# Kernel tuning notes

Hardware: AMD Instinct MI355X
Metric: run time of the kernel (lower is better)

## Reference

```python
import math
import jax, jax.numpy as jnp
import numpy as np

BLOCK = 32          # MRA block size (fixed to 32 by the CUDA kernels)
NUM_HEADS = 12
HEAD_DIM = 64
NUM_BLOCKS = 512    # top-k blocks kept per (batch*head) row
FIRST_N = 0         # initial_prior_first_n_blocks
DIAG_N = 3          # initial_prior_diagonal_n_blocks


def _low_res_logit(q, k, v, mask):
    # q,k,v: (B, S, D); mask: (B, S)
    B, S, D = q.shape
    nb = S // BLOCK
    tc = mask.reshape(B, nb, BLOCK).sum(-1)            # token count per block
    denom = tc[:, :, None] + 1e-6
    q_hat = q.reshape(B, nb, BLOCK, D).sum(2) / denom
    k_hat = k.reshape(B, nb, BLOCK, D).sum(2) / denom
    v_hat = v.reshape(B, nb, BLOCK, D).sum(2) / denom
    logit = jnp.einsum('bnd,bmd->bnm', q_hat, k_hat) / math.sqrt(D)
    row_max = logit.max(-1, keepdims=True)             # before mask penalty, as in torch
    logit = logit - 1e4 * ((tc[:, None, :] * tc[:, :, None]) < 0.5).astype(logit.dtype)
    return logit, tc, row_max, v_hat


def _block_idxes(lrl):
    # lrl: (B, nb, nb) normalized low-res logits (stop-gradient'ed by caller)
    B, nb, _ = lrl.shape
    if DIAG_N > 0:
        off = DIAG_N // 2
        r = jnp.arange(nb)
        diag = (jnp.abs(r[:, None] - r[None, :]) <= off).astype(lrl.dtype)
        lrl = lrl + diag[None] * 5000.0
    if FIRST_N > 0:
        lrl = lrl.at[:, :FIRST_N, :].add(5000.0)
        lrl = lrl.at[:, :, :FIRST_N].add(5000.0)
    vals, idx = jax.lax.top_k(lrl.reshape(B, -1), NUM_BLOCKS)
    thresh = vals.min(-1)
    hi_mask = (lrl >= thresh[:, None, None]).astype(lrl.dtype)
    return idx, hi_mask


def mra2_attention(q, k, v, mask):
    # q,k,v: (meta_batch, S, D); mask: (meta_batch, S). approx_mode == 'full'.
    B, S, D = q.shape
    nb = S // BLOCK
    q = q * mask[:, :, None]
    k = k * mask[:, :, None]
    v = v * mask[:, :, None]
    lrl, tc, row_max, v_hat = _low_res_logit(q, k, v, mask)
    idx, hi_mask = _block_idxes(jax.lax.stop_gradient(lrl - row_max))
    qi = idx // nb                                     # (B, NUM_BLOCKS) query block id
    ki = idx % nb                                      # (B, NUM_BLOCKS) key block id
    b_ix = jnp.arange(B)[:, None]
    # mm_to_sparse: gather blocks, block layout is (key_pos, query_pos) as in the CUDA kernel
    qb = q.reshape(B, nb, BLOCK, D)[b_ix, qi]          # (B, NB, 32, D)
    kb = k.reshape(B, nb, BLOCK, D)[b_ix, ki]
    hr_logit = jnp.einsum('bnkd,bnqd->bnkq', kb, qb) / math.sqrt(D)
    # sparse_max: per-query-row max over all selected blocks in that row
    idx_vals = hr_logit.max(-2)                        # (B, NB, 32q)
    max_vals = jnp.full((B, nb, BLOCK), -1e9, hr_logit.dtype).at[b_ix, qi].max(idx_vals)
    hr_logit = hr_logit - max_vals[b_ix, qi][:, :, None, :]
    # sparse_mask over key positions of each selected block
    mk = mask.reshape(B, nb, BLOCK)[b_ix, ki]          # (B, NB, 32k)
    hr_logit = hr_logit - 1e4 * (1.0 - mk)[:, :, :, None]
    hr_attn = jnp.exp(hr_logit)
    # sparse_dense_mm: scatter-add block contributions back to query rows
    vb = v.reshape(B, nb, BLOCK, D)[b_ix, ki]
    out_blk = jnp.einsum('bnkq,bnkd->bnqd', hr_attn, vb)
    hr_out = jnp.zeros((B, nb, BLOCK, D), q.dtype).at[b_ix, qi].add(out_blk).reshape(B, S, D)
    hr_norm = jnp.zeros((B, nb, BLOCK), q.dtype).at[b_ix, qi].add(hr_attn.sum(-2)).reshape(B, S)
    max_vals_flat = max_vals.reshape(B, S)
    # low-resolution branch (approx_mode == 'full')
    lr_attn = jnp.exp(lrl - row_max - 1e4 * hi_mask) * tc[:, None, :]
    lr_out = jnp.broadcast_to(
        jnp.einsum('bnm,bmd->bnd', lr_attn, v_hat)[:, :, None, :], (B, nb, BLOCK, D)
    ).reshape(B, S, D)
    lr_norm = jnp.broadcast_to(lr_attn.sum(-1)[:, :, None], (B, nb, BLOCK)).reshape(B, S)
    log_corr = (jnp.broadcast_to(row_max, (B, nb, BLOCK)).reshape(B, S) - max_vals_flat) * mask
    lr_corr = jnp.exp(log_corr * (log_corr <= 0).astype(log_corr.dtype))
    hr_corr = jnp.exp(-log_corr * (log_corr > 0).astype(log_corr.dtype))
    num = hr_out * hr_corr[:, :, None] + lr_out * lr_corr[:, :, None]
    den = hr_norm * hr_corr + lr_norm * lr_corr + 1e-6
    ctx = num / den[:, :, None]
    return ctx * mask[:, :, None]


def setup_inputs() -> dict:
    key = jax.random.key(0)
    ks = jax.random.split(key, 4)
    B, S, H = 4, 4096, 768
    return {
        'hidden_states': jax.random.normal(ks[0], (B, S, H), jnp.float32),
        'attention_mask': jnp.zeros((B, S), jnp.float32),  # extended mask form (0 == keep)
        'Wq': jax.random.normal(ks[1], (H, H), jnp.float32) * 0.02,
        'bq': jnp.zeros((H,), jnp.float32),
        'Wk': jax.random.normal(ks[2], (H, H), jnp.float32) * 0.02,
        'bk': jnp.zeros((H,), jnp.float32),
        'Wv': jax.random.normal(ks[3], (H, H), jnp.float32) * 0.02,
        'bv': jnp.zeros((H,), jnp.float32),
    }


def reference(hidden_states, attention_mask, Wq, bq, Wk, bk, Wv, bv):
    B, S, H = hidden_states.shape

    def heads(x):  # (B,S,H) -> (B*nh, S, hd)
        return x.reshape(B, S, NUM_HEADS, HEAD_DIM).transpose(0, 2, 1, 3).reshape(B * NUM_HEADS, S, HEAD_DIM)

    q = heads(hidden_states @ Wq.T + bq)
    k = heads(hidden_states @ Wk.T + bk)
    v = heads(hidden_states @ Wv.T + bv)
    # revert get_extended_attention_mask: (1 - m) * -10000 -> m
    mask = 1.0 + attention_mask / 10000.0
    mask = jnp.broadcast_to(mask[:, None, :], (B, NUM_HEADS, S)).reshape(B * NUM_HEADS, S)
    ctx = mra2_attention(q, k, v, mask)
    return ctx.reshape(B, NUM_HEADS, S, HEAD_DIM).transpose(0, 2, 1, 3).reshape(B, S, H)
```

## Files before the change

kernel.cpp:

```cpp
#include <hip/hip_runtime.h>
#include <math.h>


#define S_LEN 4096
#define NBLK  128
#define BHT   48
#define HD    64

typedef __attribute__((ext_vector_type(8))) short bf16x8;
typedef __attribute__((ext_vector_type(4))) float f32x4;
typedef unsigned short u16;
typedef unsigned int   u32;
typedef unsigned long long u64;

__device__ __forceinline__ u16 bf16rne(float x) {
    u32 u = __float_as_uint(x);
    u32 r = u + 0x7FFFu + ((u >> 16) & 1u);
    return (u16)(r >> 16);
}
__device__ __forceinline__ float b2f(u16 h) {
    return __uint_as_float((u32)h << 16);
}

__device__ __forceinline__ void gload_lds16(const void* g, void* l) {
    __builtin_amdgcn_global_load_lds((const __attribute__((address_space(1))) void*)g,
                                     (__attribute__((address_space(3))) void*)l, 16, 0, 0);
}

#define NX8 (16384 * 768 / 8)
#define NW8 (768 * 768 / 8)

__global__ __launch_bounds__(256) void split_all(
    const float* __restrict__ X,
    const float* __restrict__ Wq, const float* __restrict__ Wk, const float* __restrict__ Wv,
    u16* __restrict__ Xh, u16* __restrict__ Xl,
    u16* __restrict__ Wh, u16* __restrict__ Wl)
{
    int i = blockIdx.x * 256 + threadIdx.x;
    if (i >= NX8 + 3 * NW8) return;
    const float* src; u16* dh; u16* dl; size_t off8;
    if (i < NX8) { src = X; dh = Xh; dl = Xl; off8 = i; }
    else {
        int j = i - NX8;
        int w = j / NW8, r = j - w * NW8;
        src = (w == 0) ? Wq : (w == 1) ? Wk : Wv;
        dh = Wh + (size_t)w * 768 * 768;
        dl = Wl + (size_t)w * 768 * 768;
        off8 = r;
    }
    const float4* xp = (const float4*)src + off8 * 2;
    float4 a = xp[0], b = xp[1];
    float xs[8] = {a.x, a.y, a.z, a.w, b.x, b.y, b.z, b.w};
    bf16x8 vh, vl;
    #pragma unroll
    for (int j = 0; j < 8; ++j) {
        u16 hh = bf16rne(xs[j]);
        float hf = b2f(hh);
        vh[j] = (short)hh;
        vl[j] = (short)bf16rne(xs[j] - hf);
    }
    *(bf16x8*)&dh[off8 * 8] = vh;
    *(bf16x8*)&dl[off8 * 8] = vl;
}

__global__ __launch_bounds__(256, 3) void qkv_mfma(
    const u16* __restrict__ Xh, const u16* __restrict__ Xl,
    const u16* __restrict__ Wh, const u16* __restrict__ Wl,
    const float* __restrict__ bq, const float* __restrict__ bk, const float* __restrict__ bv,
    const float* __restrict__ am,
    u16* __restrict__ Qh, u16* __restrict__ Ql,
    u16* __restrict__ Kh, u16* __restrict__ Kl,
    u16* __restrict__ Vth, u16* __restrict__ Vtl)
{
    const int wg = blockIdx.x;
    const int logical = (wg & 7) * 288 + (wg >> 3);
    const int mt = logical / 18;
    const int rr = logical - mt * 18;
    const int nt = rr % 6;
    const int z  = rr / 6;

    const float* bias = (z == 0) ? bq : (z == 1) ? bk : bv;
    const u16* Wzh = Wh + (size_t)z * 768 * 768;
    const u16* Wzl = Wl + (size_t)z * 768 * 768;
    const int m0 = mt * 128, n0 = nt * 128;

    __shared__ char smem[32768];
    const int tid  = threadIdx.x;
    const int lane = tid & 63;
    const int w    = tid >> 6;
    const int wm   = (w >> 1) * 64, wn = (w & 1) * 64;

    const int rbase = (w < 2) ? m0 : n0;
    const int sub0  = (w & 1) * 4;
    char* ldsdst    = (w < 2) ? smem : (smem + 16384);
    const int srow = lane >> 2;
    const int scg  = (lane & 3) ^ ((lane >> 3) & 3);
    const int tslot = (lane & 15) * 4 + ((lane >> 4) ^ ((lane >> 1) & 3));

    f32x4 acc[4][4];
    #pragma unroll
    for (int i = 0; i < 4; ++i)
        #pragma unroll
        for (int j = 0; j < 4; ++j) acc[i][j] = (f32x4){0.f, 0.f, 0.f, 0.f};

    for (int k0 = 0; k0 < 2304; k0 += 64) {
        const u16* srcA = (k0 < 1536) ? Xh : Xl;
        const u16* srcB = (k0 < 768) ? Wzh : ((k0 < 1536) ? Wzl : Wzh);
        const int  kk   = (k0 < 768) ? k0 : ((k0 < 1536) ? (k0 - 768) : (k0 - 1536));
        const u16* src  = (w < 2) ? srcA : srcB;
        __syncthreads();
        #pragma unroll
        for (int h = 0; h < 2; ++h)
            #pragma unroll
            for (int i = 0; i < 4; ++i) {
                int sub = sub0 + i;
                const u16* g = src + (size_t)(rbase + sub * 16 + srow) * 768
                                   + (kk + h * 32 + scg * 8);
                gload_lds16(g, ldsdst + (h * 8 + sub) * 1024);
            }
        __syncthreads();

        #pragma unroll
        for (int h = 0; h < 2; ++h) {
            bf16x8 af[4], bf[4];
            #pragma unroll
            for (int f = 0; f < 4; ++f) {
                af[f] = *(const bf16x8*)&smem[(h * 8 + (w >> 1) * 4 + f) * 1024 + tslot * 16];
                bf[f] = *(const bf16x8*)&smem[16384 + (h * 8 + (w & 1) * 4 + f) * 1024 + tslot * 16];
            }
            #pragma unroll
            for (int i = 0; i < 4; ++i)
                #pragma unroll
                for (int j = 0; j < 4; ++j)
                    acc[i][j] = __builtin_amdgcn_mfma_f32_16x16x32_bf16(af[i], bf[j], acc[i][j], 0, 0, 0);
        }
    }

    if (z < 2) {
        u16* Ph = (z == 0) ? Qh : Kh;
        u16* Pl = (z == 0) ? Ql : Kl;
        const float qscale = (z == 0) ? 0.125f : 1.0f;
        #pragma unroll
        for (int i = 0; i < 4; ++i) {
            #pragma unroll
            for (int j = 0; j < 4; ++j) {
                int col = n0 + wn + j * 16 + (lane & 15);
                int h = col >> 6, d = col & 63;
                float bsv = bias[col];
                #pragma unroll
                for (int r = 0; r < 4; ++r) {
                    int row = m0 + wm + i * 16 + (lane >> 4) * 4 + r;
                    int b = row >> 12, s = row & 4095;
                    float mv = 1.0f + am[row] * 1e-4f;
                    float e = (acc[i][j][r] + bsv) * mv * qscale;
                    u16 hh = bf16rne(e);
                    u16 ll = bf16rne(e - b2f(hh));
                    size_t a = (((size_t)(b * 12 + h)) * S_LEN + s) * HD + d;
                    Ph[a] = hh; Pl[a] = ll;
                }
            }
        }
    } else {
        u32* buf = (u32*)smem;
        const int bb = m0 >> 12;
        #pragma unroll
        for (int p = 0; p < 4; ++p) {
            const int hh_ = p & 1;
            const int rh  = p >> 1;
            __syncthreads();
            if (((w & 1) == hh_) && ((w >> 1) == rh)) {
                #pragma unroll
                for (int i = 0; i < 4; ++i) {
                    #pragma unroll
                    for (int j = 0; j < 4; ++j) {
                        int d_local = j * 16 + (lane & 15);
                        int col = n0 + hh_ * 64 + d_local;
                        float bsv = bias[col];
                        #pragma unroll
                        for (int r = 0; r < 4; ++r) {
                            int s_local = i * 16 + (lane >> 4) * 4 + r;
                            float mv = 1.0f + am[m0 + rh * 64 + s_local] * 1e-4f;
                            float e = (acc[i][j][r] + bsv) * mv;
                            u16 h16 = bf16rne(e);
                            u16 l16 = bf16rne(e - b2f(h16));
                            buf[d_local * 66 + s_local] = ((u32)h16 << 16) | (u32)l16;
                        }
                    }
                }
            }
            __syncthreads();
            int d_local = tid >> 2;
            int s_chunk = (tid & 3) * 16;
            int head = (n0 >> 6) + hh_;
            size_t ob = (((size_t)(bb * 12 + head)) * HD + d_local) * S_LEN
                        + (m0 & 4095) + rh * 64 + s_chunk;
            #pragma unroll
            for (int gq = 0; gq < 2; ++gq) {
                bf16x8 vh8, vl8;
                #pragma unroll
                for (int t = 0; t < 8; ++t) {
                    u32 pk = buf[d_local * 66 + s_chunk + gq * 8 + t];
                    vh8[t] = (short)(pk >> 16);
                    vl8[t] = (short)(pk & 0xFFFF);
                }
                *(bf16x8*)&Vth[ob + gq * 8] = vh8;
                *(bf16x8*)&Vtl[ob + gq * 8] = vl8;
            }
        }
    }
}

__global__ __launch_bounds__(256) void hsum_kernel(
    const float* __restrict__ X, const float* __restrict__ am,
    double* __restrict__ hsum, double* __restrict__ tcd)
{
    int blk = blockIdx.x & 127, b = blockIdx.x >> 7;
    int tid = threadIdx.x;
    const float* xb  = X  + ((size_t)(b * S_LEN + blk * 32)) * 768;
    const float* amb = am + b * S_LEN + blk * 32;
    for (int d = tid; d < 768; d += 256) {
        double s = 0.0;
        for (int t = 0; t < 32; ++t)
            s += (double)xb[(size_t)t * 768 + d] * (1.0 + (double)amb[t] * 1e-4);
        hsum[(size_t)blockIdx.x * 768 + d] = s;
    }
    if (tid == 0) {
        double t = 0.0;
        for (int i = 0; i < 32; ++i) t += 1.0 + (double)amb[i] * 1e-4;
        tcd[blockIdx.x] = t;
    }
}

__global__ __launch_bounds__(256) void ghat_kernel(
    const double* __restrict__ hsum,
    const float* __restrict__ Wq, const float* __restrict__ Wk,
    const float* __restrict__ bq, const float* __restrict__ bk,
    const double* __restrict__ tcd,
    double* __restrict__ qhat, double* __restrict__ khat)
{
    const float* W; const float* bias; double* outp;
    if (blockIdx.z == 0) { W = Wq; bias = bq; outp = qhat; }
    else                 { W = Wk; bias = bk; outp = khat; }
    const int n0 = blockIdx.x * 64, m0 = blockIdx.y * 64;
    __shared__ double As[16][72];
    __shared__ float  Bs[16][72];
    const int tid = threadIdx.x;
    const int tx = tid & 15, ty = tid >> 4;
    double acc[4][4] = {};
    const int lr = tid >> 2, lc = (tid & 3) * 4;
    for (int k0 = 0; k0 < 768; k0 += 16) {
        double a0 = hsum[(size_t)(m0 + lr) * 768 + k0 + lc + 0];
        double a1 = hsum[(size_t)(m0 + lr) * 768 + k0 + lc + 1];
        double a2 = hsum[(size_t)(m0 + lr) * 768 + k0 + lc + 2];
        double a3 = hsum[(size_t)(m0 + lr) * 768 + k0 + lc + 3];
        float4 bv = *(const float4*)&W[(size_t)(n0 + lr) * 768 + k0 + lc];
        __syncthreads();
        As[lc+0][lr] = a0; As[lc+1][lr] = a1; As[lc+2][lr] = a2; As[lc+3][lr] = a3;
        Bs[lc+0][lr] = bv.x; Bs[lc+1][lr] = bv.y; Bs[lc+2][lr] = bv.z; Bs[lc+3][lr] = bv.w;
        __syncthreads();
        #pragma unroll
        for (int kk = 0; kk < 16; ++kk) {
            double af[4]; float bf[4];
            #pragma unroll
            for (int i = 0; i < 4; ++i) af[i] = As[kk][ty*4+i];
            #pragma unroll
            for (int j = 0; j < 4; ++j) bf[j] = Bs[kk][tx*4+j];
            #pragma unroll
            for (int i = 0; i < 4; ++i)
                #pragma unroll
                for (int j = 0; j < 4; ++j)
                    acc[i][j] += af[i] * (double)bf[j];
        }
    }
    #pragma unroll
    for (int i = 0; i < 4; ++i) {
        int m = m0 + ty*4 + i;
        int b = m >> 7, blk = m & 127;
        double t = tcd[m];
        #pragma unroll
        for (int j = 0; j < 4; ++j) {
            int o = n0 + tx*4 + j;
            int h = o >> 6, d = o & 63;
            outp[(((size_t)(b*12 + h)) * NBLK + blk) * HD + d] = (acc[i][j] + t * (double)bias[o]) / (t + 1e-6);
        }
    }
}

__global__ __launch_bounds__(128) void lrl_kernel(
    const double* __restrict__ qhat, const double* __restrict__ khat,
    const double* __restrict__ tcd,
    double* __restrict__ lrl, double* __restrict__ rmax,
    u64* __restrict__ keys)
{
    const int qi = blockIdx.x, bh = blockIdx.y;
    const int b = bh / 12;
    __shared__ double qr[64];
    __shared__ double red[128];
    const int tid = threadIdx.x;
    if (tid < 64) qr[tid] = qhat[(((size_t)bh) * NBLK + qi) * HD + tid];
    __syncthreads();
    const double* kr = &khat[(((size_t)bh) * NBLK + tid) * HD];
    double s = 0.0;
    #pragma unroll
    for (int d = 0; d < 64; d += 2) {
        double2 kv2 = *(const double2*)&kr[d];
        s += qr[d] * kv2.x + qr[d + 1] * kv2.y;
    }
    s *= 0.125;
    red[tid] = s;
    __syncthreads();
    for (int off = 64; off > 0; off >>= 1) {
        if (tid < off) red[tid] = fmax(red[tid], red[tid + off]);
        __syncthreads();
    }
    const double rmaxv = red[0];
    double pen = (tcd[b * NBLK + qi] * tcd[b * NBLK + tid] < 0.5) ? 1e4 : 0.0;
    const double lv = s - pen;
    lrl[(size_t)bh * (NBLK*NBLK) + (size_t)qi * NBLK + tid] = lv;
    if (tid == 0) rmax[bh * NBLK + qi] = rmaxv;
    int dd = qi - tid; if (dd < 0) dd = -dd;
    double ks_ = lv - rmaxv + ((dd <= 1) ? 5000.0 : 0.0);
    u64 u = (u64)__double_as_longlong(ks_);
    u = (u >> 63) ? ~u : (u | 0x8000000000000000ULL);
    keys[(size_t)bh * (NBLK*NBLK) + (size_t)qi * NBLK + tid] = u;
}

__global__ __launch_bounds__(64) void vhat_kernel(
    const u16* __restrict__ Vth, const u16* __restrict__ Vtl,
    const double* __restrict__ tcd,
    float* __restrict__ vhat, float* __restrict__ tcf)
{
    const int d = blockIdx.x, bh = blockIdx.y;
    const int b = bh / 12;
    const int l = threadIdx.x;
    const u16* ph = Vth + ((size_t)bh * HD + d) * S_LEN + l * 64;
    const u16* pl = Vtl + ((size_t)bh * HD + d) * S_LEN + l * 64;
    float s[2] = {0.f, 0.f};
    #pragma unroll
    for (int g = 0; g < 2; ++g) {
        #pragma unroll
        for (int v = 0; v < 4; ++v) {
            bf16x8 vh = *(const bf16x8*)&ph[g * 32 + v * 8];
            bf16x8 vl = *(const bf16x8*)&pl[g * 32 + v * 8];
            #pragma unroll
            for (int j = 0; j < 8; ++j)
                s[g] += b2f((u16)vh[j]) + b2f((u16)vl[j]);
        }
    }
    #pragma unroll
    for (int g = 0; g < 2; ++g) {
        int blk = l * 2 + g;
        float tc = (float)tcd[b * NBLK + blk];
        vhat[(((size_t)bh) * NBLK + blk) * HD + d] = s[g] / (tc + 1e-6f);
        if (d == 0) tcf[bh * NBLK + blk] = tc;
    }
}

__global__ __launch_bounds__(256) void topk_kernel(
    const u64* __restrict__ keys,
    double* __restrict__ th64, int* __restrict__ cnt, unsigned char* __restrict__ lists,
    int* __restrict__ eqbuf, int* __restrict__ eqcnt)
{
    const int bh = blockIdx.x, tid = threadIdx.x;
    const int wid = tid >> 6;
    __shared__ int hist[4][256];
    __shared__ u64 s_pref;
    __shared__ int s_K;
    const u64* kp = keys + (size_t)bh * (NBLK*NBLK);
    if (tid < 128) cnt[bh * NBLK + tid] = 0;
    if (tid == 0) eqcnt[bh] = 0;

    u64 pref = 0, pmask = 0;
    int K = 512;
    for (int by = 7; by >= 0; --by) {
        #pragma unroll
        for (int w = 0; w < 4; ++w) hist[w][tid] = 0;
        __syncthreads();
        for (int i = tid; i < NBLK*NBLK; i += 256) {
            u64 u = kp[i];
            if ((u & pmask) == pref)
                atomicAdd(&hist[wid][(int)((u >> (by*8)) & 255)], 1);
        }
        __syncthreads();
        int tot = hist[0][tid] + hist[1][tid] + hist[2][tid] + hist[3][tid];
        hist[0][tid] = tot;
        __syncthreads();
        if (tid == 0) {
            int c = 0, bsel = 0;
            for (int x = 255; x >= 0; --x) {
                if (c + hist[0][x] >= K) { bsel = x; break; }
                c += hist[0][x];
            }
            s_pref = pref | ((u64)bsel << (by*8));
            s_K = K - c;
        }
        __syncthreads();
        pref = s_pref; K = s_K;
        pmask |= 0xFFULL << (by*8);
        __syncthreads();
    }
    const u64 tkey = pref;
    int n_take = K;
    if (tid == 0) {
        u64 u = (tkey & 0x8000000000000000ULL) ? (tkey ^ 0x8000000000000000ULL) : ~tkey;
        th64[bh] = __longlong_as_double((long long)u);
    }
    for (int i = tid; i < NBLK*NBLK; i += 256) {
        u64 u = kp[i];
        if (u > tkey) {
            int qi = i >> 7, ki = i & 127;
            int pos = atomicAdd(&cnt[bh * NBLK + qi], 1);
            lists[(((size_t)bh) * NBLK + qi) * NBLK + pos] = (unsigned char)ki;
        } else if (u == tkey) {
            int e = atomicAdd(&eqcnt[bh], 1);
            if (e < 512) eqbuf[bh * 512 + e] = i;
        }
    }
    __syncthreads();
    if (tid == 0) {
        int ne = eqcnt[bh]; if (ne > 512) ne = 512;
        int* eb = &eqbuf[bh * 512];
        for (int a = 1; a < ne; ++a) {
            int v = eb[a]; int x = a - 1;
            while (x >= 0 && eb[x] > v) { eb[x+1] = eb[x]; --x; }
            eb[x+1] = v;
        }
        if (n_take > ne) n_take = ne;
        for (int j = 0; j < n_take; ++j) {
            int i = eb[j]; int qi = i >> 7, ki = i & 127;
            int pos = cnt[bh * NBLK + qi]++;
            lists[(((size_t)bh) * NBLK + qi) * NBLK + pos] = (unsigned char)ki;
        }
    }
    __syncthreads();
    if (tid < 128) {
        int n = cnt[bh * NBLK + tid];
        unsigned char* l = &lists[(((size_t)bh) * NBLK + tid) * NBLK];
        for (int a = 1; a < n; ++a) {
            unsigned char v = l[a]; int x = a - 1;
            while (x >= 0 && l[x] > v) { l[x+1] = l[x]; --x; }
            l[x+1] = v;
        }
    }
}

__global__ __launch_bounds__(64) void hr_mfma(
    const u16* __restrict__ Qh, const u16* __restrict__ Ql,
    const u16* __restrict__ Kh, const u16* __restrict__ Kl,
    const u16* __restrict__ Vth, const u16* __restrict__ Vtl,
    const double* __restrict__ lrl64, const double* __restrict__ rmax64, const double* __restrict__ th64,
    const int* __restrict__ cnt, const unsigned char* __restrict__ lists,
    const float* __restrict__ vhat, const float* __restrict__ tcf,
    const float* __restrict__ am, float* __restrict__ out)
{
    const int qi = blockIdx.x, bh = blockIdx.y;
    const int l  = threadIdx.x;
    const int lr_ = l & 15, lg = l >> 4;
    __shared__ u16 PhL[32][40];
    __shared__ u16 PlL[32][40];
    __shared__ float wlr[128];
    __shared__ float lrvec[64];

    bf16x8 qfh[2][2], qfl[2][2];
    #pragma unroll
    for (int qs = 0; qs < 2; ++qs)
        #pragma unroll
        for (int ds = 0; ds < 2; ++ds) {
            size_t a = (((size_t)bh) * S_LEN + qi * 32 + qs * 16 + lr_) * HD + ds * 32 + lg * 8;
            qfh[qs][ds] = *(const bf16x8*)&Qh[a];
            qfl[qs][ds] = *(const bf16x8*)&Ql[a];
        }

    float m_run[2][4], l_run[2][4];
    f32x4 oacc[2][4];
    #pragma unroll
    for (int qs = 0; qs < 2; ++qs) {
        #pragma unroll
        for (int r = 0; r < 4; ++r) { m_run[qs][r] = -1e30f; l_run[qs][r] = 0.f; }
        #pragma unroll
        for (int dv = 0; dv < 4; ++dv) oacc[qs][dv] = (f32x4){0.f, 0.f, 0.f, 0.f};
    }

    const int c = cnt[bh * NBLK + qi];
    const unsigned char* ml = &lists[(((size_t)bh) * NBLK + qi) * NBLK];

    for (int bi = 0; bi < c; ++bi) {
        const int ki = ml[bi];
        f32x4 S[2][2];
        #pragma unroll
        for (int qs = 0; qs < 2; ++qs)
            #pragma unroll
            for (int ks = 0; ks < 2; ++ks) S[qs][ks] = (f32x4){0.f, 0.f, 0.f, 0.f};
        #pragma unroll
        for (int ds = 0; ds < 2; ++ds)
            #pragma unroll
            for (int ks = 0; ks < 2; ++ks) {
                size_t a = (((size_t)bh) * S_LEN + ki * 32 + ks * 16 + lr_) * HD + ds * 32 + lg * 8;
                bf16x8 kh = *(const bf16x8*)&Kh[a];
                bf16x8 kl = *(const bf16x8*)&Kl[a];
                S[0][ks] = __builtin_amdgcn_mfma_f32_16x16x32_bf16(qfh[0][ds], kh, S[0][ks], 0, 0, 0);
                S[1][ks] = __builtin_amdgcn_mfma_f32_16x16x32_bf16(qfh[1][ds], kh, S[1][ks], 0, 0, 0);
                S[0][ks] = __builtin_amdgcn_mfma_f32_16x16x32_bf16(qfh[0][ds], kl, S[0][ks], 0, 0, 0);
                S[1][ks] = __builtin_amdgcn_mfma_f32_16x16x32_bf16(qfh[1][ds], kl, S[1][ks], 0, 0, 0);
                S[0][ks] = __builtin_amdgcn_mfma_f32_16x16x32_bf16(qfl[0][ds], kh, S[0][ks], 0, 0, 0);
                S[1][ks] = __builtin_amdgcn_mfma_f32_16x16x32_bf16(qfl[1][ds], kh, S[1][ks], 0, 0, 0);
            }
        #pragma unroll
        for (int qs = 0; qs < 2; ++qs)
            #pragma unroll
            for (int r = 0; r < 4; ++r) {
                float bm = fmaxf(S[qs][0][r], S[qs][1][r]);
                bm = fmaxf(bm, __shfl_xor(bm, 1));
                bm = fmaxf(bm, __shfl_xor(bm, 2));
                bm = fmaxf(bm, __shfl_xor(bm, 4));
                bm = fmaxf(bm, __shfl_xor(bm, 8));
                float mn = fmaxf(m_run[qs][r], bm);
                float sc = expf(m_run[qs][r] - mn);
                m_run[qs][r] = mn;
                float p0 = expf(S[qs][0][r] - mn);
                float p1 = expf(S[qs][1][r] - mn);
                float rs = p0 + p1;
                rs += __shfl_xor(rs, 1);
                rs += __shfl_xor(rs, 2);
                rs += __shfl_xor(rs, 4);
                rs += __shfl_xor(rs, 8);
                l_run[qs][r] = l_run[qs][r] * sc + rs;
                #pragma unroll
                for (int dv = 0; dv < 4; ++dv) oacc[qs][dv][r] *= sc;
                int row = qs * 16 + lg * 4 + r;
                u16 h0 = bf16rne(p0); u16 lo0 = bf16rne(p0 - b2f(h0));
                u16 h1 = bf16rne(p1); u16 lo1 = bf16rne(p1 - b2f(h1));
                PhL[row][lr_]      = h0;  PlL[row][lr_]      = lo0;
                PhL[row][16 + lr_] = h1;  PlL[row][16 + lr_] = lo1;
            }
        __syncthreads();
        bf16x8 pah[2], pal[2];
        #pragma unroll
        for (int qs = 0; qs < 2; ++qs) {
            pah[qs] = *(const bf16x8*)&PhL[qs * 16 + lr_][lg * 8];
            pal[qs] = *(const bf16x8*)&PlL[qs * 16 + lr_][lg * 8];
        }
        #pragma unroll
        for (int dv = 0; dv < 4; ++dv) {
            size_t a = (((size_t)bh) * HD + dv * 16 + lr_) * S_LEN + ki * 32 + lg * 8;
            bf16x8 vh = *(const bf16x8*)&Vth[a];
            bf16x8 vl = *(const bf16x8*)&Vtl[a];
            #pragma unroll
            for (int qs = 0; qs < 2; ++qs) {
                oacc[qs][dv] = __builtin_amdgcn_mfma_f32_16x16x32_bf16(pah[qs], vh, oacc[qs][dv], 0, 0, 0);
                oacc[qs][dv] = __builtin_amdgcn_mfma_f32_16x16x32_bf16(pah[qs], vl, oacc[qs][dv], 0, 0, 0);
                oacc[qs][dv] = __builtin_amdgcn_mfma_f32_16x16x32_bf16(pal[qs], vh, oacc[qs][dv], 0, 0, 0);
            }
        }
        __syncthreads();
    }

    const double thv  = th64[bh];
    const double rm64 = rmax64[bh * NBLK + qi];
    const int b = bh / 12, h = bh % 12;
    float wpair = 0.f;
    #pragma unroll
    for (int half = 0; half < 2; ++half) {
        int m = l + half * 64;
        double lv = lrl64[(size_t)bh * (NBLK*NBLK) + (size_t)qi * NBLK + m];
        int dd = qi - m; if (dd < 0) dd = -dd;
        double s = lv - rm64 + ((dd <= 1) ? 5000.0 : 0.0);
        float wv;
        if (s >= thv) wv = 0.f;
        else          wv = (float)exp(lv - rm64) * tcf[bh * NBLK + m];
        wlr[m] = wv;
        wpair += wv;
    }
    float s_lrn = wpair;
    s_lrn += __shfl_xor(s_lrn, 1);
    s_lrn += __shfl_xor(s_lrn, 2);
    s_lrn += __shfl_xor(s_lrn, 4);
    s_lrn += __shfl_xor(s_lrn, 8);
    s_lrn += __shfl_xor(s_lrn, 16);
    s_lrn += __shfl_xor(s_lrn, 32);
    __syncthreads();
    float a_ = 0.f;
    for (int m = 0; m < 128; ++m)
        a_ += wlr[m] * vhat[(((size_t)bh) * NBLK + m) * HD + l];
    lrvec[l] = a_;
    __syncthreads();
    float lv4[4];
    #pragma unroll
    for (int dv = 0; dv < 4; ++dv) lv4[dv] = lrvec[dv * 16 + lr_];

    const float rmf = (float)rm64;
    #pragma unroll
    for (int qs = 0; qs < 2; ++qs)
        #pragma unroll
        for (int r = 0; r < 4; ++r) {
            int q = qs * 16 + lg * 4 + r;
            int srow = qi * 32 + q;
            float mv = 1.0f + am[b * S_LEN + srow] * 1e-4f;
            float logc = (rmf - m_run[qs][r]) * mv;
            float lrc = (logc <= 0.f) ? expf(logc)  : 1.0f;
            float hrc = (logc >  0.f) ? expf(-logc) : 1.0f;
            float den = l_run[qs][r] * hrc + s_lrn * lrc + 1e-6f;
            float scd = mv / den;
            size_t ob = ((size_t)(b * S_LEN + srow)) * 768 + h * HD;
            #pragma unroll
            for (int dv = 0; dv < 4; ++dv)
                out[ob + dv * 16 + lr_] = (oacc[qs][dv][r] * hrc + lv4[dv] * lrc) * scd;
        }
}

extern "C" void kernel_launch(void* const* d_in, const int* in_sizes, int n_in,
                              void* d_out, int out_size, void* d_ws, size_t ws_size,
                              hipStream_t stream)
{
    (void)in_sizes; (void)n_in; (void)out_size; (void)ws_size;
    const float* X  = (const float*)d_in[0];
    const float* am = (const float*)d_in[1];
    const float* Wq = (const float*)d_in[2];
    const float* bq = (const float*)d_in[3];
    const float* Wk = (const float*)d_in[4];
    const float* bk = (const float*)d_in[5];
    const float* Wv = (const float*)d_in[6];
    const float* bv = (const float*)d_in[7];
    float* out = (float*)d_out;

    char* p = (char*)d_ws;
    const size_t PLANE = (size_t)BHT * S_LEN * HD * 2;
    u16* Qh  = (u16*)p; p += PLANE;
    u16* Ql  = (u16*)p; p += PLANE;
    u16* Kh  = (u16*)p; p += PLANE;
    u16* Kl  = (u16*)p; p += PLANE;
    u16* Vth = (u16*)p; p += PLANE;
    u16* Vtl = (u16*)p; p += PLANE;
    char* region = p;

    char* pa = region;
    u16* Xh = (u16*)pa; pa += (size_t)16384 * 768 * 2;
    u16* Xl = (u16*)pa; pa += (size_t)16384 * 768 * 2;
    u16* Wh = (u16*)pa; pa += (size_t)3 * 768 * 768 * 2;
    u16* Wl = (u16*)pa; pa += (size_t)3 * 768 * 768 * 2;

    char* pb = region;
    double* hsum   = (double*)pb; pb += (size_t)512 * 768 * 8;
    double* tcd    = (double*)pb; pb += (size_t)512 * 8;
    double* qhat64 = (double*)pb; pb += (size_t)BHT * NBLK * HD * 8;
    double* khat64 = (double*)pb; pb += (size_t)BHT * NBLK * HD * 8;
    double* lrl64  = (double*)pb; pb += (size_t)BHT * NBLK * NBLK * 8;
    double* rmax64 = (double*)pb; pb += (size_t)BHT * NBLK * 8;
    double* th64   = (double*)pb; pb += (size_t)BHT * 8;
    u64* keys   = (u64*)pb;   pb += (size_t)BHT * NBLK * NBLK * 8;
    float* vhat = (float*)pb; pb += (size_t)BHT * NBLK * HD * 4;
    float* tcf  = (float*)pb; pb += (size_t)BHT * NBLK * 4;
    int* cnt    = (int*)pb;   pb += (size_t)BHT * NBLK * 4;
    int* eqbuf  = (int*)pb;   pb += (size_t)BHT * 512 * 4;
    int* eqcnt  = (int*)pb;   pb += (size_t)BHT * 4;
    unsigned char* lists = (unsigned char*)pb; pb += (size_t)BHT * NBLK * NBLK;

    split_all<<<7008, 256, 0, stream>>>(X, Wq, Wk, Wv, Xh, Xl, Wh, Wl);
    qkv_mfma<<<2304, 256, 0, stream>>>(Xh, Xl, Wh, Wl, bq, bk, bv, am,
                                       Qh, Ql, Kh, Kl, Vth, Vtl);

    hsum_kernel<<<512, 256, 0, stream>>>(X, am, hsum, tcd);
    ghat_kernel<<<dim3(12, 8, 2), 256, 0, stream>>>(hsum, Wq, Wk, bq, bk, tcd, qhat64, khat64);
    lrl_kernel<<<dim3(128, BHT), 128, 0, stream>>>(qhat64, khat64, tcd, lrl64, rmax64, keys);
    vhat_kernel<<<dim3(64, BHT), 64, 0, stream>>>(Vth, Vtl, tcd, vhat, tcf);
    topk_kernel<<<BHT, 256, 0, stream>>>(keys, th64, cnt, lists, eqbuf, eqcnt);

    hr_mfma<<<dim3(NBLK, BHT), 64, 0, stream>>>(Qh, Ql, Kh, Kl, Vth, Vtl,
                                                lrl64, rmax64, th64,
                                                cnt, lists, vhat, tcf, am, out);
}
```

Before: 704.0 us.

## Double-buffer QKV GEMM loads, batch four query rows in lrl, lazy softmax rescale

The QKV MFMA GEMM now uses a two-stage LDS double buffer with 32-wide k steps, so the next tile's global-to-LDS load overlaps the current MFMAs and there is one barrier per step. The low-res logit kernel processes four query blocks per workgroup, reusing each khat row load across four dot products, and the grid shrinks accordingly. The sparse attention kernel only rescales the running max and accumulators when the block max exceeds the running max by more than 8, which skips most exp and multiply work. That lazy rescale lets probabilities grow up to about e^8 before renormalising, which slightly changes the numerics.

```diff
diff --git a/kernel.cpp b/kernel.cpp
--- a/kernel.cpp
+++ b/kernel.cpp
@@ -92,7 +92,6 @@
 
     const int rbase = (w < 2) ? m0 : n0;
     const int sub0  = (w & 1) * 4;
-    char* ldsdst    = (w < 2) ? smem : (smem + 16384);
     const int srow = lane >> 2;
     const int scg  = (lane & 3) ^ ((lane >> 3) & 3);
     const int tslot = (lane & 15) * 4 + ((lane >> 4) ^ ((lane >> 1) & 3));
@@ -103,37 +102,39 @@
         #pragma unroll
         for (int j = 0; j < 4; ++j) acc[i][j] = (f32x4){0.f, 0.f, 0.f, 0.f};
 
-    for (int k0 = 0; k0 < 2304; k0 += 64) {
+    auto STAGE = [&](int buf, int t) {
+        const int k0 = t * 32;
         const u16* srcA = (k0 < 1536) ? Xh : Xl;
         const u16* srcB = (k0 < 768) ? Wzh : ((k0 < 1536) ? Wzl : Wzh);
         const int  kk   = (k0 < 768) ? k0 : ((k0 < 1536) ? (k0 - 768) : (k0 - 1536));
         const u16* src  = (w < 2) ? srcA : srcB;
-        __syncthreads();
-        #pragma unroll
-        for (int h = 0; h < 2; ++h)
-            #pragma unroll
-            for (int i = 0; i < 4; ++i) {
-                int sub = sub0 + i;
-                const u16* g = src + (size_t)(rbase + sub * 16 + srow) * 768
-                                   + (kk + h * 32 + scg * 8);
-                gload_lds16(g, ldsdst + (h * 8 + sub) * 1024);
-            }
-        __syncthreads();
-
-        #pragma unroll
-        for (int h = 0; h < 2; ++h) {
-            bf16x8 af[4], bf[4];
-            #pragma unroll
-            for (int f = 0; f < 4; ++f) {
-                af[f] = *(const bf16x8*)&smem[(h * 8 + (w >> 1) * 4 + f) * 1024 + tslot * 16];
-                bf[f] = *(const bf16x8*)&smem[16384 + (h * 8 + (w & 1) * 4 + f) * 1024 + tslot * 16];
-            }
-            #pragma unroll
-            for (int i = 0; i < 4; ++i)
-                #pragma unroll
-                for (int j = 0; j < 4; ++j)
-                    acc[i][j] = __builtin_amdgcn_mfma_f32_16x16x32_bf16(af[i], bf[j], acc[i][j], 0, 0, 0);
-        }
+        char* dst = smem + buf * 16384 + ((w < 2) ? 0 : 8192);
+        #pragma unroll
+        for (int i = 0; i < 4; ++i) {
+            const u16* g = src + (size_t)(rbase + (sub0 + i) * 16 + srow) * 768 + (kk + scg * 8);
+            gload_lds16(g, dst + (sub0 + i) * 1024);
+        }
+    };
+
+    STAGE(0, 0);
+    __syncthreads();
+    int cur = 0;
+    for (int t = 0; t < 72; ++t) {
+        if (t + 1 < 72) STAGE(cur ^ 1, t + 1);
+        const char* bufp = smem + cur * 16384;
+        bf16x8 af[4], bf[4];
+        #pragma unroll
+        for (int f = 0; f < 4; ++f) {
+            af[f] = *(const bf16x8*)&bufp[((w >> 1) * 4 + f) * 1024 + tslot * 16];
+            bf[f] = *(const bf16x8*)&bufp[8192 + ((w & 1) * 4 + f) * 1024 + tslot * 16];
+        }
+        #pragma unroll
+        for (int i = 0; i < 4; ++i)
+            #pragma unroll
+            for (int j = 0; j < 4; ++j)
+                acc[i][j] = __builtin_amdgcn_mfma_f32_16x16x32_bf16(af[i], bf[j], acc[i][j], 0, 0, 0);
+        __syncthreads();
+        cur ^= 1;
     }
 
     if (z < 2) {
@@ -292,37 +293,51 @@
     double* __restrict__ lrl, double* __restrict__ rmax,
     u64* __restrict__ keys)
 {
-    const int qi = blockIdx.x, bh = blockIdx.y;
+    const int q0 = blockIdx.x * 4, bh = blockIdx.y;
     const int b = bh / 12;
-    __shared__ double qr[64];
-    __shared__ double red[128];
+    __shared__ double qr[4][64];
+    __shared__ double red[4][128];
     const int tid = threadIdx.x;
-    if (tid < 64) qr[tid] = qhat[(((size_t)bh) * NBLK + qi) * HD + tid];
+    if (tid < 64) {
+        #pragma unroll
+        for (int qq = 0; qq < 4; ++qq)
+            qr[qq][tid] = qhat[(((size_t)bh) * NBLK + q0 + qq) * HD + tid];
+    }
     __syncthreads();
     const double* kr = &khat[(((size_t)bh) * NBLK + tid) * HD];
-    double s = 0.0;
-    #pragma unroll
+    double s[4] = {0.0, 0.0, 0.0, 0.0};
     for (int d = 0; d < 64; d += 2) {
         double2 kv2 = *(const double2*)&kr[d];
-        s += qr[d] * kv2.x + qr[d + 1] * kv2.y;
-    }
-    s *= 0.125;
-    red[tid] = s;
+        #pragma unroll
+        for (int qq = 0; qq < 4; ++qq)
+            s[qq] += qr[qq][d] * kv2.x + qr[qq][d + 1] * kv2.y;
+    }
+    #pragma unroll
+    for (int qq = 0; qq < 4; ++qq) { s[qq] *= 0.125; red[qq][tid] = s[qq]; }
     __syncthreads();
     for (int off = 64; off > 0; off >>= 1) {
-        if (tid < off) red[tid] = fmax(red[tid], red[tid + off]);
-        __syncthreads();
-    }
-    const double rmaxv = red[0];
-    double pen = (tcd[b * NBLK + qi] * tcd[b * NBLK + tid] < 0.5) ? 1e4 : 0.0;
-    const double lv = s - pen;
-    lrl[(size_t)bh * (NBLK*NBLK) + (size_t)qi * NBLK + tid] = lv;
-    if (tid == 0) rmax[bh * NBLK + qi] = rmaxv;
-    int dd = qi - tid; if (dd < 0) dd = -dd;
-    double ks_ = lv - rmaxv + ((dd <= 1) ? 5000.0 : 0.0);
-    u64 u = (u64)__double_as_longlong(ks_);
-    u = (u >> 63) ? ~u : (u | 0x8000000000000000ULL);
-    keys[(size_t)bh * (NBLK*NBLK) + (size_t)qi * NBLK + tid] = u;
+        if (tid < off) {
+            #pragma unroll
+            for (int qq = 0; qq < 4; ++qq)
+                red[qq][tid] = fmax(red[qq][tid], red[qq][tid + off]);
+        }
+        __syncthreads();
+    }
+    const double tck = tcd[b * NBLK + tid];
+    #pragma unroll
+    for (int qq = 0; qq < 4; ++qq) {
+        const int qi = q0 + qq;
+        const double rmaxv = red[qq][0];
+        double pen = (tcd[b * NBLK + qi] * tck < 0.5) ? 1e4 : 0.0;
+        const double lv = s[qq] - pen;
+        lrl[(size_t)bh * (NBLK*NBLK) + (size_t)qi * NBLK + tid] = lv;
+        if (tid == 0) rmax[bh * NBLK + qi] = rmaxv;
+        int dd = qi - tid; if (dd < 0) dd = -dd;
+        double ks_ = lv - rmaxv + ((dd <= 1) ? 5000.0 : 0.0);
+        u64 u = (u64)__double_as_longlong(ks_);
+        u = (u >> 63) ? ~u : (u | 0x8000000000000000ULL);
+        keys[(size_t)bh * (NBLK*NBLK) + (size_t)qi * NBLK + tid] = u;
+    }
 }
 
 __global__ __launch_bounds__(64) void vhat_kernel(
@@ -514,19 +529,21 @@
                 bm = fmaxf(bm, __shfl_xor(bm, 2));
                 bm = fmaxf(bm, __shfl_xor(bm, 4));
                 bm = fmaxf(bm, __shfl_xor(bm, 8));
-                float mn = fmaxf(m_run[qs][r], bm);
-                float sc = expf(m_run[qs][r] - mn);
-                m_run[qs][r] = mn;
-                float p0 = expf(S[qs][0][r] - mn);
-                float p1 = expf(S[qs][1][r] - mn);
+                if (bm > m_run[qs][r] + 8.f) {
+                    float sc = expf(m_run[qs][r] - bm);
+                    m_run[qs][r] = bm;
+                    l_run[qs][r] *= sc;
+                    #pragma unroll
+                    for (int dv = 0; dv < 4; ++dv) oacc[qs][dv][r] *= sc;
+                }
+                float p0 = expf(S[qs][0][r] - m_run[qs][r]);
+                float p1 = expf(S[qs][1][r] - m_run[qs][r]);
                 float rs = p0 + p1;
                 rs += __shfl_xor(rs, 1);
                 rs += __shfl_xor(rs, 2);
                 rs += __shfl_xor(rs, 4);
                 rs += __shfl_xor(rs, 8);
-                l_run[qs][r] = l_run[qs][r] * sc + rs;
-                #pragma unroll
-                for (int dv = 0; dv < 4; ++dv) oacc[qs][dv][r] *= sc;
+                l_run[qs][r] += rs;
                 int row = qs * 16 + lg * 4 + r;
                 u16 h0 = bf16rne(p0); u16 lo0 = bf16rne(p0 - b2f(h0));
                 u16 h1 = bf16rne(p1); u16 lo1 = bf16rne(p1 - b2f(h1));
@@ -661,7 +678,7 @@
 
     hsum_kernel<<<512, 256, 0, stream>>>(X, am, hsum, tcd);
     ghat_kernel<<<dim3(12, 8, 2), 256, 0, stream>>>(hsum, Wq, Wk, bq, bk, tcd, qhat64, khat64);
-    lrl_kernel<<<dim3(128, BHT), 128, 0, stream>>>(qhat64, khat64, tcd, lrl64, rmax64, keys);
+    lrl_kernel<<<dim3(32, BHT), 128, 0, stream>>>(qhat64, khat64, tcd, lrl64, rmax64, keys);
     vhat_kernel<<<dim3(64, BHT), 64, 0, stream>>>(Vth, Vtl, tcd, vhat, tcf);
     topk_kernel<<<BHT, 256, 0, stream>>>(keys, th64, cnt, lists, eqbuf, eqcnt);
 
```

After: 949.3 us. 34.8% more time.
